# Kernel optimization log

Measured on AMD Instinct MI355X. Metric: run time of the kernel, lower is better.

## Reference

```python
import jax, jax.numpy as jnp
import numpy as np

COMMITMENT_COST = 0.25


def setup_inputs() -> dict:
    key = jax.random.key(0)
    k1, k2 = jax.random.split(key)
    inputs = jax.random.normal(k1, (16, 4096, 256), dtype=jnp.float32)
    codewords = jax.random.normal(k2, (1024, 256), dtype=jnp.float32)
    return {"inputs": inputs, "codewords": codewords}


def reference(inputs, codewords):
    # inputs: (*, D), codewords: (K, D)
    D = codewords.shape[-1]
    flat = inputs.reshape(-1, D)  # (N, D)
    x_sq = jnp.sum(flat * flat, axis=-1, keepdims=True)            # (N, 1)
    c_sq = jnp.sum(codewords * codewords, axis=-1)                 # (K,)
    distances = x_sq - 2.0 * (flat @ codewords.T) + c_sq           # (N, K)
    encoding_indices = jnp.argmin(distances, axis=1)               # (N,)
    quantized = codewords[encoding_indices].reshape(inputs.shape)  # (*, D)
    # Straight-through estimator
    quantized_st = inputs + jax.lax.stop_gradient(quantized - inputs)
    quantizing_loss = jnp.mean((quantized_st - jax.lax.stop_gradient(inputs)) ** 2)
    commitment_loss = jnp.mean((jax.lax.stop_gradient(quantized_st) - inputs) ** 2)
    loss = quantizing_loss + COMMITMENT_COST * commitment_loss
    return quantized_st, encoding_indices.reshape(inputs.shape[:-1]), loss
```

## Files before the change

kernel.cpp:

```cpp
#include <hip/hip_runtime.h>
#include <math.h>

typedef _Float16 v8h __attribute__((ext_vector_type(8)));
typedef float v4f __attribute__((ext_vector_type(4)));

constexpr int D      = 256;
constexpr int NTILE  = 64;
constexpr int KS     = 8;
constexpr int TILE_B = 8192;
constexpr int TPW    = 4;
constexpr int WIN_B  = 32768;
constexpr int NWIN   = 16;
#define GUARD 2.0f

__global__ void vq_prep(const float* __restrict__ cw, unsigned short* __restrict__ img) {
    int gid = blockIdx.x * 256 + threadIdx.x;
    int t  = gid >> 9;
    int r  = gid & 511;
    int ks = r >> 6;
    int l  = r & 63;
    int cand = t * 16 + (l & 15);
    int k0   = ks * 32 + (l >> 4) * 8;
    const float* src = cw + (size_t)cand * D + k0;
    float4 t0 = *(const float4*)(src);
    float4 t1 = *(const float4*)(src + 4);
    v8h h;
    h[0] = (_Float16)t0.x; h[1] = (_Float16)t0.y;
    h[2] = (_Float16)t0.z; h[3] = (_Float16)t0.w;
    h[4] = (_Float16)t1.x; h[5] = (_Float16)t1.y;
    h[6] = (_Float16)t1.z; h[7] = (_Float16)t1.w;
    *(v8h*)((char*)img + (size_t)gid * 16) = h;
}

__global__ void vq_csq(const float* __restrict__ cw, float* __restrict__ csq) {
    int k = blockIdx.x * blockDim.x + threadIdx.x;
    const float4* p = reinterpret_cast<const float4*>(cw + (size_t)k * D);
    float s = 0.f;
    #pragma unroll 8
    for (int i = 0; i < D / 4; ++i) {
        float4 v = p[i];
        s += v.x * v.x; s += v.y * v.y; s += v.z * v.z; s += v.w * v.w;
    }
    csq[k] = s;
}

__launch_bounds__(256, 2)
__global__ void vq_main(const float* __restrict__ inp,
                        const float* __restrict__ cw,
                        const unsigned short* __restrict__ img,
                        const float* __restrict__ csq,
                        float* __restrict__ outq,
                        float* __restrict__ outi,
                        float* __restrict__ bsum) {
    __shared__ __align__(16) char smem[2][WIN_B];
    __shared__ int4  s_pack[128];
    __shared__ float s_xsq[128];
    __shared__ int   s_win[128];
    __shared__ float s_l[4];

    const int tid  = threadIdx.x;
    const int lane = tid & 63;
    const int w    = tid >> 6;
    const int lr   = lane & 15;
    const int q    = lane >> 4;
    const int base = blockIdx.x * 128 + w * 32;

    #pragma unroll
    for (int i = 0; i < 8; ++i) {
        int off = i * 4096 + w * 1024;
        __builtin_amdgcn_global_load_lds(
            (const __attribute__((address_space(1))) unsigned int*)((const char*)img + off + lane * 16),
            (__attribute__((address_space(3))) unsigned int*)(&smem[0][off]),
            16, 0, 0);
    }

    v8h a2[2][8];
    #pragma unroll
    for (int m = 0; m < 2; ++m) {
        const float* rp = inp + (size_t)(base + m * 16 + lr) * D + q * 8;
        float sq = 0.f;
        #pragma unroll
        for (int ks = 0; ks < KS; ++ks) {
            float4 t0 = *(const float4*)(rp + ks * 32);
            float4 t1 = *(const float4*)(rp + ks * 32 + 4);
            sq = fmaf(t0.x, t0.x, sq); sq = fmaf(t0.y, t0.y, sq);
            sq = fmaf(t0.z, t0.z, sq); sq = fmaf(t0.w, t0.w, sq);
            sq = fmaf(t1.x, t1.x, sq); sq = fmaf(t1.y, t1.y, sq);
            sq = fmaf(t1.z, t1.z, sq); sq = fmaf(t1.w, t1.w, sq);
            v8h h;
            h[0] = (_Float16)(-2.f * t0.x); h[1] = (_Float16)(-2.f * t0.y);
            h[2] = (_Float16)(-2.f * t0.z); h[3] = (_Float16)(-2.f * t0.w);
            h[4] = (_Float16)(-2.f * t1.x); h[5] = (_Float16)(-2.f * t1.y);
            h[6] = (_Float16)(-2.f * t1.z); h[7] = (_Float16)(-2.f * t1.w);
            a2[m][ks] = h;
        }
        sq += __shfl_xor(sq, 16);
        sq += __shfl_xor(sq, 32);
        if (q == 0) s_xsq[w * 32 + m * 16 + lr] = sq;
    }

    const float BIGF = __uint_as_float(0x7F000000u);
    float v1[2][4], v2[2][4];
    #pragma unroll
    for (int m = 0; m < 2; ++m)
        #pragma unroll
        for (int r = 0; r < 4; ++r) { v1[m][r] = BIGF; v2[m][r] = BIGF; }

    asm volatile("s_waitcnt vmcnt(0)" ::: "memory");
    __builtin_amdgcn_s_barrier();
    __builtin_amdgcn_sched_barrier(0);

    int cur = 0;
    for (int win = 0; win < NWIN; ++win) {
        if (win + 1 < NWIN) {
            const char* srct = (const char*)img + (size_t)(win + 1) * WIN_B;
            #pragma unroll
            for (int i = 0; i < 8; ++i) {
                int off = i * 4096 + w * 1024;
                __builtin_amdgcn_global_load_lds(
                    (const __attribute__((address_space(1))) unsigned int*)(srct + off + lane * 16),
                    (__attribute__((address_space(3))) unsigned int*)(&smem[cur ^ 1][off]),
                    16, 0, 0);
            }
        }

        const char* bb = smem[cur];
        v4f acc[TPW][2];
        #pragma unroll
        for (int tt = 0; tt < TPW; ++tt) {
            float cq = csq[(win * TPW + tt) * 16 + lr] + 4096.f;
            v4f c = {cq, cq, cq, cq};
            acc[tt][0] = c; acc[tt][1] = c;
        }
        #pragma unroll
        for (int ks = 0; ks < KS; ++ks) {
            v8h b0 = *(const v8h*)(bb + 0 * TILE_B + ks * 1024 + lane * 16);
            v8h b1 = *(const v8h*)(bb + 1 * TILE_B + ks * 1024 + lane * 16);
            v8h b2 = *(const v8h*)(bb + 2 * TILE_B + ks * 1024 + lane * 16);
            v8h b3 = *(const v8h*)(bb + 3 * TILE_B + ks * 1024 + lane * 16);
            acc[0][0] = __builtin_amdgcn_mfma_f32_16x16x32_f16(a2[0][ks], b0, acc[0][0], 0, 0, 0);
            acc[1][0] = __builtin_amdgcn_mfma_f32_16x16x32_f16(a2[0][ks], b1, acc[1][0], 0, 0, 0);
            acc[2][0] = __builtin_amdgcn_mfma_f32_16x16x32_f16(a2[0][ks], b2, acc[2][0], 0, 0, 0);
            acc[3][0] = __builtin_amdgcn_mfma_f32_16x16x32_f16(a2[0][ks], b3, acc[3][0], 0, 0, 0);
            acc[0][1] = __builtin_amdgcn_mfma_f32_16x16x32_f16(a2[1][ks], b0, acc[0][1], 0, 0, 0);
            acc[1][1] = __builtin_amdgcn_mfma_f32_16x16x32_f16(a2[1][ks], b1, acc[1][1], 0, 0, 0);
            acc[2][1] = __builtin_amdgcn_mfma_f32_16x16x32_f16(a2[1][ks], b2, acc[2][1], 0, 0, 0);
            acc[3][1] = __builtin_amdgcn_mfma_f32_16x16x32_f16(a2[1][ks], b3, acc[3][1], 0, 0, 0);
        }
        #pragma unroll
        for (int tt = 0; tt < TPW; ++tt) {
            unsigned idx = (unsigned)((win * TPW + tt) * 16) | (unsigned)lr;
            #pragma unroll
            for (int m = 0; m < 2; ++m)
                #pragma unroll
                for (int r = 0; r < 4; ++r) {
                    float f = __uint_as_float(((__float_as_uint(acc[tt][m][r]) + 0x200u) & 0xFFFFFC00u) | idx);
                    float mx = fmaxf(v1[m][r], f);
                    v2[m][r] = fminf(v2[m][r], mx);
                    v1[m][r] = fminf(v1[m][r], f);
                }
        }

        asm volatile("s_waitcnt vmcnt(0)" ::: "memory");
        __builtin_amdgcn_s_barrier();
        __builtin_amdgcn_sched_barrier(0);
        cur ^= 1;
    }

    #pragma unroll
    for (int m = 0; m < 2; ++m)
        #pragma unroll
        for (int r = 0; r < 4; ++r) {
            float L0 = v1[m][r], L1 = v2[m][r], L2 = BIGF, L3 = BIGF;
            #pragma unroll
            for (int off = 8; off; off >>= 1) {
                float P0 = __shfl_xor(L0, off, 16);
                float P1 = __shfl_xor(L1, off, 16);
                float P2 = __shfl_xor(L2, off, 16);
                float P3 = __shfl_xor(L3, off, 16);
                float M0 = fminf(L0, P3), M1 = fminf(L1, P2);
                float M2 = fminf(L2, P1), M3 = fminf(L3, P0);
                float a0 = fminf(M0, M2), c0 = fmaxf(M0, M2);
                float b0 = fminf(M1, M3), d0 = fmaxf(M1, M3);
                L0 = fminf(a0, b0); L1 = fmaxf(a0, b0);
                L2 = fminf(c0, d0); L3 = fmaxf(c0, d0);
            }
            if (lr == 0) {
                int rloc = m * 16 + q * 4 + r;
                s_pack[w * 32 + rloc] = make_int4(
                    (int)__float_as_uint(L0), (int)__float_as_uint(L1),
                    (int)__float_as_uint(L2), (int)__float_as_uint(L3));
            }
        }

    const int c = lane & 3;
    float lacc = 0.f;
    #pragma unroll
    for (int h = 0; h < 2; ++h) {
        int rloc = h * 16 + (lane >> 2);
        int grow = base + rloc;
        int4 pk = s_pack[w * 32 + rloc];
        float L0 = __uint_as_float((unsigned)pk.x);
        float L1 = __uint_as_float((unsigned)pk.y);
        float L2 = __uint_as_float((unsigned)pk.z);
        float L3 = __uint_as_float((unsigned)pk.w);
        float xq = s_xsq[w * 32 + rloc];

        int   bi;
        float bd;
        bool rescue = (L1 - L0) < GUARD;
        if (rescue) {
            float Lc = (c == 0) ? L0 : (c == 1) ? L1 : (c == 2) ? L2 : L3;
            int cd = (int)(__float_as_uint(Lc) & 1023u);
            const float4* xp = (const float4*)(inp + (size_t)grow * D);
            const float4* cp = (const float4*)(cw + (size_t)cd * D);
            float dot = 0.f, xsq = 0.f;
            #pragma unroll 8
            for (int i = 0; i < D / 4; ++i) {
                float4 xv = xp[i];
                float4 cv = cp[i];
                xsq = fmaf(xv.x, xv.x, xsq);
                xsq = fmaf(xv.y, xv.y, xsq);
                xsq = fmaf(xv.z, xv.z, xsq);
                xsq = fmaf(xv.w, xv.w, xsq);
                dot = fmaf(xv.x, cv.x, dot);
                dot = fmaf(xv.y, cv.y, dot);
                dot = fmaf(xv.z, cv.z, dot);
                dot = fmaf(xv.w, cv.w, dot);
            }
            float m2 = dot + dot;
            float t  = xsq - m2;
            float e  = t + csq[cd];
            bd = e; bi = cd;
            #pragma unroll
            for (int off = 1; off <= 2; off <<= 1) {
                float ev = __shfl_xor(bd, off, 4);
                int   iv = __shfl_xor(bi, off, 4);
                bool  tk = (ev < bd) || (ev == bd && iv < bi);
                bd = tk ? ev : bd;
                bi = tk ? iv : bi;
            }
        } else {
            bi = (int)(__float_as_uint(L0) & 1023u);
            bd = (L0 - 4096.f) + xq;
        }

        if (c == 0) { s_win[w * 32 + rloc] = bi; lacc += bd; }
    }

    #pragma unroll 4
    for (int rr = 0; rr < 32; ++rr) {
        int bw = s_win[w * 32 + rr];
        float4 cv = *(const float4*)(cw + (size_t)bw * D + lane * 4);
        *(float4*)(outq + (size_t)(base + rr) * D + lane * 4) = cv;
        if (lane == 0) outi[base + rr] = (float)bw;
    }

    #pragma unroll
    for (int off = 32; off; off >>= 1) lacc += __shfl_xor(lacc, off);
    if (lane == 0) s_l[w] = lacc;
    __syncthreads();
    if (tid == 0) bsum[blockIdx.x] = s_l[0] + s_l[1] + s_l[2] + s_l[3];
}

__global__ void vq_finalize(const float* __restrict__ bsum, float* __restrict__ out_loss,
                            int nb, float scale) {
    __shared__ float s[4];
    int tid = threadIdx.x;
    float v = 0.f;
    for (int i = tid; i < nb; i += 256) v += bsum[i];
    #pragma unroll
    for (int off = 32; off; off >>= 1) v += __shfl_down(v, off, 64);
    if ((tid & 63) == 0) s[tid >> 6] = v;
    __syncthreads();
    if (tid == 0) out_loss[0] = (s[0] + s[1] + s[2] + s[3]) * scale;
}

extern "C" void kernel_launch(void* const* d_in, const int* in_sizes, int n_in,
                              void* d_out, int out_size, void* d_ws, size_t ws_size,
                              hipStream_t stream) {
    const float* inp = (const float*)d_in[0];
    const float* cw  = (const float*)d_in[1];
    float* out = (float*)d_out;
    const int N = in_sizes[0] / D;
    const int K = in_sizes[1] / D;

    char* ws = (char*)d_ws;
    unsigned short* img = (unsigned short*)ws;
    float* csq  = (float*)(ws + (size_t)K * D * 2);
    float* bsum = csq + K;

    float* outq = out;
    float* outi = out + (size_t)N * D;
    float* outl = outi + N;

    vq_prep<<<dim3((K * 32) / 256), dim3(256), 0, stream>>>(cw, img);
    vq_csq<<<dim3(K / 256), dim3(256), 0, stream>>>(cw, csq);

    vq_main<<<dim3(N / 128), dim3(256), 0, stream>>>(inp, cw, img, csq,
                                                     outq, outi, bsum);
    vq_finalize<<<dim3(1), dim3(256), 0, stream>>>(bsum, outl, N / 128,
                                                   1.25f / ((float)N * (float)D));
}
```

Measured before the change: 90.64 us.

## Use 512-thread blocks with 8-tile codebook windows and LDS-cached norms

```diff
diff --git a/kernel.cpp b/kernel.cpp
--- a/kernel.cpp
+++ b/kernel.cpp
@@ -5,13 +5,12 @@
 typedef float v4f __attribute__((ext_vector_type(4)));
 
 constexpr int D      = 256;
-constexpr int NTILE  = 64;
 constexpr int KS     = 8;
 constexpr int TILE_B = 8192;
-constexpr int TPW    = 4;
-constexpr int WIN_B  = 32768;
-constexpr int NWIN   = 16;
-#define GUARD 2.0f
+constexpr int TPW    = 8;
+constexpr int WIN_B  = 65536;
+constexpr int NWIN   = 8;
+#define GUARD 1.0f
 
 __global__ void vq_prep(const float* __restrict__ cw, unsigned short* __restrict__ img) {
     int gid = blockIdx.x * 256 + threadIdx.x;
@@ -44,7 +43,7 @@
     csq[k] = s;
 }
 
-__launch_bounds__(256, 2)
+__launch_bounds__(512, 2)
 __global__ void vq_main(const float* __restrict__ inp,
                         const float* __restrict__ cw,
                         const unsigned short* __restrict__ img,
@@ -53,25 +52,38 @@
                         float* __restrict__ outi,
                         float* __restrict__ bsum) {
     __shared__ __align__(16) char smem[2][WIN_B];
-    __shared__ int4  s_pack[128];
-    __shared__ float s_xsq[128];
-    __shared__ int   s_win[128];
-    __shared__ float s_l[4];
+    __shared__ float s_cq[1024];
+    __shared__ int4  s_pack[256];
+    __shared__ float s_xsq[256];
+    __shared__ int   s_win[256];
+    __shared__ float s_l[8];
 
     const int tid  = threadIdx.x;
     const int lane = tid & 63;
     const int w    = tid >> 6;
     const int lr   = lane & 15;
     const int q    = lane >> 4;
-    const int base = blockIdx.x * 128 + w * 32;
-
-    #pragma unroll
-    for (int i = 0; i < 8; ++i) {
-        int off = i * 4096 + w * 1024;
-        __builtin_amdgcn_global_load_lds(
-            (const __attribute__((address_space(1))) unsigned int*)((const char*)img + off + lane * 16),
-            (__attribute__((address_space(3))) unsigned int*)(&smem[0][off]),
-            16, 0, 0);
+    const int base = blockIdx.x * 256 + w * 32;
+
+#define VQ_STAGE(WIN, BUF)                                                           \
+    {                                                                                \
+        const char* srct = (const char*)img + (size_t)(WIN) * WIN_B;                 \
+        _Pragma("unroll")                                                            \
+        for (int i = 0; i < 8; ++i) {                                                \
+            int off = i * 8192 + w * 1024;                                           \
+            __builtin_amdgcn_global_load_lds(                                        \
+                (const __attribute__((address_space(1))) unsigned int*)(srct + off + lane * 16), \
+                (__attribute__((address_space(3))) unsigned int*)(&smem[BUF][off]),  \
+                16, 0, 0);                                                           \
+        }                                                                            \
+    }
+
+    VQ_STAGE(0, 0)
+
+    {
+        float2 cv2 = ((const float2*)csq)[tid];
+        s_cq[tid * 2 + 0] = cv2.x + 4096.f;
+        s_cq[tid * 2 + 1] = cv2.y + 4096.f;
     }
 
     v8h a2[2][8];
@@ -106,47 +118,35 @@
         #pragma unroll
         for (int r = 0; r < 4; ++r) { v1[m][r] = BIGF; v2[m][r] = BIGF; }
 
-    asm volatile("s_waitcnt vmcnt(0)" ::: "memory");
-    __builtin_amdgcn_s_barrier();
-    __builtin_amdgcn_sched_barrier(0);
+    __syncthreads();
 
     int cur = 0;
     for (int win = 0; win < NWIN; ++win) {
-        if (win + 1 < NWIN) {
-            const char* srct = (const char*)img + (size_t)(win + 1) * WIN_B;
-            #pragma unroll
-            for (int i = 0; i < 8; ++i) {
-                int off = i * 4096 + w * 1024;
-                __builtin_amdgcn_global_load_lds(
-                    (const __attribute__((address_space(1))) unsigned int*)(srct + off + lane * 16),
-                    (__attribute__((address_space(3))) unsigned int*)(&smem[cur ^ 1][off]),
-                    16, 0, 0);
-            }
-        }
+        if (win + 1 < NWIN) VQ_STAGE(win + 1, cur ^ 1)
 
         const char* bb = smem[cur];
         v4f acc[TPW][2];
         #pragma unroll
         for (int tt = 0; tt < TPW; ++tt) {
-            float cq = csq[(win * TPW + tt) * 16 + lr] + 4096.f;
+            float cq = s_cq[(win * TPW + tt) * 16 + lr];
             v4f c = {cq, cq, cq, cq};
             acc[tt][0] = c; acc[tt][1] = c;
         }
+        __builtin_amdgcn_s_setprio(1);
         #pragma unroll
         for (int ks = 0; ks < KS; ++ks) {
-            v8h b0 = *(const v8h*)(bb + 0 * TILE_B + ks * 1024 + lane * 16);
-            v8h b1 = *(const v8h*)(bb + 1 * TILE_B + ks * 1024 + lane * 16);
-            v8h b2 = *(const v8h*)(bb + 2 * TILE_B + ks * 1024 + lane * 16);
-            v8h b3 = *(const v8h*)(bb + 3 * TILE_B + ks * 1024 + lane * 16);
-            acc[0][0] = __builtin_amdgcn_mfma_f32_16x16x32_f16(a2[0][ks], b0, acc[0][0], 0, 0, 0);
-            acc[1][0] = __builtin_amdgcn_mfma_f32_16x16x32_f16(a2[0][ks], b1, acc[1][0], 0, 0, 0);
-            acc[2][0] = __builtin_amdgcn_mfma_f32_16x16x32_f16(a2[0][ks], b2, acc[2][0], 0, 0, 0);
-            acc[3][0] = __builtin_amdgcn_mfma_f32_16x16x32_f16(a2[0][ks], b3, acc[3][0], 0, 0, 0);
-            acc[0][1] = __builtin_amdgcn_mfma_f32_16x16x32_f16(a2[1][ks], b0, acc[0][1], 0, 0, 0);
-            acc[1][1] = __builtin_amdgcn_mfma_f32_16x16x32_f16(a2[1][ks], b1, acc[1][1], 0, 0, 0);
-            acc[2][1] = __builtin_amdgcn_mfma_f32_16x16x32_f16(a2[1][ks], b2, acc[2][1], 0, 0, 0);
-            acc[3][1] = __builtin_amdgcn_mfma_f32_16x16x32_f16(a2[1][ks], b3, acc[3][1], 0, 0, 0);
-        }
+            v8h b[TPW];
+            #pragma unroll
+            for (int tt = 0; tt < TPW; ++tt)
+                b[tt] = *(const v8h*)(bb + tt * TILE_B + ks * 1024 + lane * 16);
+            #pragma unroll
+            for (int tt = 0; tt < TPW; ++tt) {
+                acc[tt][0] = __builtin_amdgcn_mfma_f32_16x16x32_f16(a2[0][ks], b[tt], acc[tt][0], 0, 0, 0);
+                acc[tt][1] = __builtin_amdgcn_mfma_f32_16x16x32_f16(a2[1][ks], b[tt], acc[tt][1], 0, 0, 0);
+            }
+        }
+        __builtin_amdgcn_s_setprio(0);
+
         #pragma unroll
         for (int tt = 0; tt < TPW; ++tt) {
             unsigned idx = (unsigned)((win * TPW + tt) * 16) | (unsigned)lr;
@@ -166,6 +166,7 @@
         __builtin_amdgcn_sched_barrier(0);
         cur ^= 1;
     }
+#undef VQ_STAGE
 
     #pragma unroll
     for (int m = 0; m < 2; ++m)
@@ -260,7 +261,12 @@
     for (int off = 32; off; off >>= 1) lacc += __shfl_xor(lacc, off);
     if (lane == 0) s_l[w] = lacc;
     __syncthreads();
-    if (tid == 0) bsum[blockIdx.x] = s_l[0] + s_l[1] + s_l[2] + s_l[3];
+    if (tid == 0) {
+        float s = 0.f;
+        #pragma unroll
+        for (int i = 0; i < 8; ++i) s += s_l[i];
+        bsum[blockIdx.x] = s;
+    }
 }
 
 __global__ void vq_finalize(const float* __restrict__ bsum, float* __restrict__ out_loss,
@@ -297,8 +303,8 @@
     vq_prep<<<dim3((K * 32) / 256), dim3(256), 0, stream>>>(cw, img);
     vq_csq<<<dim3(K / 256), dim3(256), 0, stream>>>(cw, csq);
 
-    vq_main<<<dim3(N / 128), dim3(256), 0, stream>>>(inp, cw, img, csq,
+    vq_main<<<dim3(N / 256), dim3(512), 0, stream>>>(inp, cw, img, csq,
                                                      outq, outi, bsum);
-    vq_finalize<<<dim3(1), dim3(256), 0, stream>>>(bsum, outl, N / 128,
+    vq_finalize<<<dim3(1), dim3(256), 0, stream>>>(bsum, outl, N / 256,
                                                    1.25f / ((float)N * (float)D));
 }
```

Measured after the change: 93.65 us. 1.03x slower.
